# Kernel tuning notes

Measured on AMD Instinct MI355X. Metric: run time of the kernel, lower is better.

The kernel has to match this reference:

```python
import jax, jax.numpy as jnp
import numpy as np

N = 100000   # nodes per graph
E = 1200000  # edges per graph
D_IN = 64
FILTERS = [128, 128, 64]
K_SLICES = 16
MLP = [32, 16, 8, 4]


def setup_inputs() -> dict:
    key = jax.random.key(0)
    ks = jax.random.split(key, 24)
    s = 0.1
    inp = {
        'x_i': jax.random.normal(ks[0], (N, D_IN), jnp.float32),
        'edge_index_i': jax.random.randint(ks[1], (2, E), 0, N, jnp.int64),
        'x_j': jax.random.normal(ks[2], (N, D_IN), jnp.float32),
        'edge_index_j': jax.random.randint(ks[3], (2, E), 0, N, jnp.int64),
    }
    # GCN conv stack params: 64->128->128->64
    dims = [D_IN] + FILTERS
    for li in range(3):
        inp[f'conv_w{li}'] = jax.random.normal(ks[4 + 2 * li], (dims[li], dims[li + 1]), jnp.float32) * s
        inp[f'conv_b{li}'] = jnp.zeros((dims[li + 1],), jnp.float32)
    d = FILTERS[-1]
    inp['att_w'] = jax.random.normal(ks[10], (d, d), jnp.float32) * s
    inp['ntn_wt'] = jax.random.normal(ks[11], (K_SLICES, d, d), jnp.float32) * s
    inp['ntn_wm'] = jax.random.normal(ks[12], (K_SLICES, 2 * d), jnp.float32) * s
    inp['ntn_b'] = jnp.zeros((K_SLICES,), jnp.float32)
    mdims = [K_SLICES] + MLP
    for li in range(4):
        inp[f'mlp_w{li}'] = jax.random.normal(ks[13 + 2 * li], (mdims[li], mdims[li + 1]), jnp.float32) * s
        inp[f'mlp_b{li}'] = jnp.zeros((mdims[li + 1],), jnp.float32)
    inp['score_w'] = jax.random.normal(ks[22], (MLP[-1], 1), jnp.float32) * s
    inp['score_b'] = jnp.zeros((1,), jnp.float32)
    return inp


def _gcn(x, W, b, src, dst):
    # PyG GCNConv: add self loops, symmetric normalization, aggregate into dst.
    n = x.shape[0]
    loop = jnp.arange(n, dtype=src.dtype)
    src = jnp.concatenate([src, loop])
    dst = jnp.concatenate([dst, loop])
    deg = jax.ops.segment_sum(jnp.ones_like(dst, dtype=x.dtype), dst, num_segments=n)
    dinv = jax.lax.rsqrt(deg)  # deg >= 1 due to self loops
    norm = dinv[src] * dinv[dst]             # [E+N]
    xw = x @ W                               # [N, Dout]
    out = jax.ops.segment_sum(xw[src] * norm[:, None], dst, num_segments=n)
    return out + b


def _attention(x, Wa):
    # global context attention pooling over nodes
    gc = jnp.tanh(jnp.mean(x @ Wa, axis=0))          # [D]
    att = jax.nn.sigmoid(x @ gc)                     # [N]
    return jnp.sum(x * att[:, None], axis=0)         # [D]


def _ntn(h_i, h_j, Wt, Wm, b):
    # s_k = h_i^T Wt[k] h_j + Wm[k] . [h_i; h_j] + b_k, then tanh
    bilinear = jnp.einsum('d,kde,e->k', h_i, Wt, h_j)
    linear = Wm @ jnp.concatenate([h_i, h_j])
    return jnp.tanh(bilinear + linear + b)           # [K]


def reference(x_i, edge_index_i, x_j, edge_index_j,
              conv_w0, conv_b0, conv_w1, conv_b1, conv_w2, conv_b2,
              att_w, ntn_wt, ntn_wm, ntn_b,
              mlp_w0, mlp_b0, mlp_w1, mlp_b1, mlp_w2, mlp_b2, mlp_w3, mlp_b3,
              score_w, score_b):
    convs = [(conv_w0, conv_b0), (conv_w1, conv_b1), (conv_w2, conv_b2)]
    si, di = edge_index_i[0], edge_index_i[1]
    sj, dj = edge_index_j[0], edge_index_j[1]
    for li, (W, b) in enumerate(convs):
        x_i = _gcn(x_i, W, b, si, di)
        x_j = _gcn(x_j, W, b, sj, dj)
        if li < len(convs) - 1:
            x_i = jax.nn.relu(x_i)
            x_j = jax.nn.relu(x_j)
    h_i = _attention(x_i, att_w)
    h_j = _attention(x_j, att_w)
    z = _ntn(h_i, h_j, ntn_wt, ntn_wm, ntn_b)        # [K]
    for W, b in [(mlp_w0, mlp_b0), (mlp_w1, mlp_b1), (mlp_w2, mlp_b2), (mlp_w3, mlp_b3)]:
        z = jax.nn.relu(z @ W + b)
    return z @ score_w + score_b                     # [1]
```

## Files before the change

kernel.cpp:

```cpp
#include <hip/hip_runtime.h>
#include <cstdint>
#include <cstddef>

#define CDIV(a,b) (((a)+(b)-1)/(b))

typedef __attribute__((ext_vector_type(8))) unsigned short ushort8v;
typedef __attribute__((ext_vector_type(8))) short short8v;
typedef __attribute__((ext_vector_type(4))) float f32x4;

constexpr int BCAP = 8192;
constexpr int CPAD = 256 * BCAP;

__device__ __forceinline__ float bf2f(unsigned short u) {
  return __uint_as_float(((unsigned)u) << 16);
}
__device__ __forceinline__ unsigned short f2bf(float f) {
  unsigned u = __float_as_uint(f);
  unsigned r = (u + 0x7fff + ((u >> 16) & 1)) >> 16;
  return (unsigned short)r;
}


__global__ void k_prep(const float* __restrict__ w0, const float* __restrict__ w1,
                       const float* __restrict__ w2,
                       unsigned short* __restrict__ w0p, unsigned short* __restrict__ w1p,
                       unsigned short* __restrict__ w2p,
                       int* __restrict__ gcur, double* __restrict__ gcsum,
                       double* __restrict__ hsum) {
  int id = blockIdx.x * 256 + threadIdx.x;
  if (id < 512) gcur[id] = 0;
  else if (id < 640) gcsum[id - 512] = 0.0;
  else if (id < 768) hsum[id - 640] = 0.0;
  if (id < 8192) {
    int k = id / 128, n = id % 128;
    w0p[n * 64 + ((((k >> 3) + n) & 7) * 8) + (k & 7)] = f2bf(w0[id]);
  }
  if (id < 16384) {
    int k = id / 128, n = id % 128;
    w1p[n * 128 + ((((k >> 3) + n) & 15) * 8) + (k & 7)] = f2bf(w1[id]);
  }
  if (id < 8192) {
    int k = id / 64, n = id % 64;
    w2p[n * 128 + ((((k >> 3) + n) & 15) * 8) + (k & 7)] = f2bf(w2[id]);
  }
}


__global__ __launch_bounds__(256) void k_place(const int* __restrict__ src0,
                                               const int* __restrict__ dst0,
                                               const int* __restrict__ src1,
                                               const int* __restrict__ dst1,
                                               int E, int N,
                                               int* __restrict__ gcur,
                                               unsigned* __restrict__ part) {
  __shared__ int bcnt[256], bbase[256], bcur[256];
  int g = blockIdx.y;
  const int* src = g ? src1 : src0;
  const int* dst = g ? dst1 : dst0;
  int t = threadIdx.x;
  int e0 = blockIdx.x * 4096, e1 = min(e0 + 4096, E);
  bcnt[t] = 0;
  __syncthreads();
  for (int e = e0 + t; e < e1; e += 256) atomicAdd(&bcnt[dst[e] >> 9], 1);
  __syncthreads();
  bbase[t] = t * BCAP + (bcnt[t] ? atomicAdd(&gcur[g * 256 + t], bcnt[t]) : 0);
  bcur[t] = 0;
  __syncthreads();
  unsigned* pg = part + (size_t)g * CPAD;
  for (int e = e0 + t; e < e1; e += 256) {
    int d = dst[e], s = src[e];
    int b = d >> 9;
    int off = atomicAdd(&bcur[b], 1);
    pg[bbase[b] + off] = ((unsigned)(d & 511) << 18) | (unsigned)(s + g * N);
  }
}


__global__ __launch_bounds__(256) void k_build(const unsigned* __restrict__ part,
                                               const int* __restrict__ gcur,
                                               int2* __restrict__ rowp2, int* __restrict__ col,
                                               float* __restrict__ dinv, int n) {
  __shared__ int cnt[512], off[512], tmp[256];
  int g = blockIdx.y, b = blockIdx.x;
  int lo = b << 9;
  if (lo >= n) return;
  int t = threadIdx.x;
  int s0 = b * BCAP;
  int cntE = gcur[g * 256 + b];
  const unsigned* pg = part + (size_t)g * CPAD;
  cnt[t] = 0; cnt[t + 256] = 0;
  __syncthreads();
  for (int e = s0 + t; e < s0 + cntE; e += 256) atomicAdd(&cnt[pg[e] >> 18], 1);
  __syncthreads();
  int a0 = cnt[2 * t], a1 = cnt[2 * t + 1];
  int ps = a0 + a1;
  tmp[t] = ps; __syncthreads();
  for (int o = 1; o < 256; o <<= 1) {
    int x = (t >= o) ? tmp[t - o] : 0;
    __syncthreads();
    tmp[t] += x;
    __syncthreads();
  }
  int ex = tmp[t] - ps;
  off[2 * t] = ex;
  off[2 * t + 1] = ex + a0;
  __syncthreads();
  for (int i = t; i < 512; i += 256) {
    int node = lo + i;
    if (node < n) {
      int st = g * CPAD + s0 + off[i];
      rowp2[g * n + node] = make_int2(st, st + cnt[i]);
      dinv[g * n + node] = rsqrtf((float)(cnt[i] + 1));
    }
  }
  __syncthreads();
  for (int e = s0 + t; e < s0 + cntE; e += 256) {
    unsigned pr = pg[e];
    int p = atomicAdd(&off[pr >> 18], 1);
    col[g * CPAD + s0 + p] = (int)(pr & 0x3FFFFu);
  }
}


__global__ void k_tobf(const float* __restrict__ in0, const float* __restrict__ in1,
                       unsigned short* __restrict__ out, int n8half, int n8) {
  int i = blockIdx.x * blockDim.x + threadIdx.x;
  if (i < n8) {
    const float4* i4 = (i < n8half) ? (const float4*)in0 : (const float4*)in1;
    int ii = (i < n8half) ? i : i - n8half;
    float4 a = i4[2 * ii], b = i4[2 * ii + 1];
    ushort8v r;
    r[0] = f2bf(a.x); r[1] = f2bf(a.y); r[2] = f2bf(a.z); r[3] = f2bf(a.w);
    r[4] = f2bf(b.x); r[5] = f2bf(b.y); r[6] = f2bf(b.z); r[7] = f2bf(b.w);
    ((ushort8v*)out)[i] = r;
  }
}


template<int D, bool OUTBF, bool ADD_BIAS, bool COLSUM>
__device__ __forceinline__ void agg_body(
    const unsigned short* __restrict__ xin, void* __restrict__ xout,
    const int2* __restrict__ rowp2, const int* __restrict__ col,
    const float* __restrict__ dinv, const float* __restrict__ bias, int n,
    float* __restrict__ partial) {
  constexpr int G = D / 8;
  constexpr int NPB = 256 / G;
  int node = blockIdx.x * NPB + threadIdx.x / G;
  int g = threadIdx.x % G;
  const ushort8v* x8 = (const ushort8v*)xin;
  float r[8];
  bool valid = node < n;
  if (valid) {
    float di = dinv[node];
    float acc[8];
    {
      ushort8v xs = x8[(size_t)node * G + g];
#pragma unroll
      for (int j = 0; j < 8; ++j) acc[j] = di * bf2f(xs[j]);
    }
    int2 rp = rowp2[node];
    int e = rp.x, e1 = rp.y;
    for (; e + 8 <= e1; e += 8) {
      int s0 = col[e], s1 = col[e + 1], s2 = col[e + 2], s3 = col[e + 3];
      int s4 = col[e + 4], s5 = col[e + 5], s6 = col[e + 6], s7 = col[e + 7];
      float w0 = dinv[s0], w1 = dinv[s1], w2 = dinv[s2], w3 = dinv[s3];
      float w4 = dinv[s4], w5 = dinv[s5], w6 = dinv[s6], w7 = dinv[s7];
      ushort8v v0 = x8[(size_t)s0 * G + g];
      ushort8v v1 = x8[(size_t)s1 * G + g];
      ushort8v v2 = x8[(size_t)s2 * G + g];
      ushort8v v3 = x8[(size_t)s3 * G + g];
      ushort8v v4 = x8[(size_t)s4 * G + g];
      ushort8v v5 = x8[(size_t)s5 * G + g];
      ushort8v v6 = x8[(size_t)s6 * G + g];
      ushort8v v7 = x8[(size_t)s7 * G + g];
#pragma unroll
      for (int j = 0; j < 8; ++j) {
        acc[j] += w0 * bf2f(v0[j]); acc[j] += w1 * bf2f(v1[j]);
        acc[j] += w2 * bf2f(v2[j]); acc[j] += w3 * bf2f(v3[j]);
        acc[j] += w4 * bf2f(v4[j]); acc[j] += w5 * bf2f(v5[j]);
        acc[j] += w6 * bf2f(v6[j]); acc[j] += w7 * bf2f(v7[j]);
      }
    }
    for (; e + 4 <= e1; e += 4) {
      int s0 = col[e], s1 = col[e + 1], s2 = col[e + 2], s3 = col[e + 3];
      float w0 = dinv[s0], w1 = dinv[s1], w2 = dinv[s2], w3 = dinv[s3];
      ushort8v v0 = x8[(size_t)s0 * G + g];
      ushort8v v1 = x8[(size_t)s1 * G + g];
      ushort8v v2 = x8[(size_t)s2 * G + g];
      ushort8v v3 = x8[(size_t)s3 * G + g];
#pragma unroll
      for (int j = 0; j < 8; ++j) {
        acc[j] += w0 * bf2f(v0[j]); acc[j] += w1 * bf2f(v1[j]);
        acc[j] += w2 * bf2f(v2[j]); acc[j] += w3 * bf2f(v3[j]);
      }
    }
    for (; e < e1; ++e) {
      int s = col[e];
      float w = dinv[s];
      ushort8v v = x8[(size_t)s * G + g];
#pragma unroll
      for (int j = 0; j < 8; ++j) acc[j] += w * bf2f(v[j]);
    }
#pragma unroll
    for (int j = 0; j < 8; ++j) {
      r[j] = di * acc[j];
      if (ADD_BIAS) r[j] += bias[g * 8 + j];
    }
    if (OUTBF) {
      ushort8v o;
#pragma unroll
      for (int j = 0; j < 8; ++j) o[j] = f2bf(r[j]);
      ((ushort8v*)xout)[(size_t)node * G + g] = o;
    } else {
      float* op = (float*)xout + (size_t)node * D + g * 8;
      *(float4*)(op + 0) = make_float4(r[0], r[1], r[2], r[3]);
      *(float4*)(op + 4) = make_float4(r[4], r[5], r[6], r[7]);
    }
  } else {
#pragma unroll
    for (int j = 0; j < 8; ++j) r[j] = 0.f;
  }
  if (COLSUM) {
    __shared__ float ws[4][64];
    int lane = threadIdx.x & 63, wave = threadIdx.x >> 6;
#pragma unroll
    for (int j = 0; j < 8; ++j) {
      float v = r[j];
      v += __shfl_xor(v, 8);
      v += __shfl_xor(v, 16);
      v += __shfl_xor(v, 32);
      r[j] = v;
    }
    if (lane < 8) {
#pragma unroll
      for (int j = 0; j < 8; ++j) ws[wave][lane * 8 + j] = r[j];
    }
    __syncthreads();
    int t = threadIdx.x;
    if (t < 64) partial[(size_t)blockIdx.x * 64 + t] = ws[0][t] + ws[1][t] + ws[2][t] + ws[3][t];
  }
}

__global__ __launch_bounds__(256) void k_aggL0(
    const unsigned short* __restrict__ x, void* __restrict__ o,
    const int2* __restrict__ rp, const int* __restrict__ col,
    const float* __restrict__ dv, int n) {
  agg_body<64, true, false, false>(x, o, rp, col, dv, nullptr, n, nullptr);
}
__global__ __launch_bounds__(256) void k_aggL1(
    const unsigned short* __restrict__ x, void* __restrict__ o,
    const int2* __restrict__ rp, const int* __restrict__ col,
    const float* __restrict__ dv, int n) {
  agg_body<128, true, false, false>(x, o, rp, col, dv, nullptr, n, nullptr);
}
__global__ __launch_bounds__(256) void k_aggF(
    const unsigned short* __restrict__ x, void* __restrict__ o,
    const int2* __restrict__ rp, const int* __restrict__ col,
    const float* __restrict__ dv, const float* __restrict__ bias, int n,
    float* __restrict__ partial) {
  agg_body<64, false, true, true>(x, o, rp, col, dv, bias, n, partial);
}


template<int K, int DOUT, bool RELU>
__device__ __forceinline__ void gemm_body(
    const unsigned short* __restrict__ A, const unsigned short* __restrict__ Wp,
    const float* __restrict__ bias, unsigned short* __restrict__ C, int n) {
  constexpr int CPR = K / 8;
  constexpr int CM = CPR - 1;
  constexpr int NT = DOUT / 16;
  __shared__ unsigned short As[128 * K];
  __shared__ unsigned short Ws[DOUT * K];
  int t = threadIdx.x;
  int blockM = blockIdx.x * 128;

#pragma unroll
  for (int id = t; id < 128 * CPR; id += 256) {
    int r = id / CPR, c = id % CPR;
    int grow = blockM + r;
    ushort8v v = {0, 0, 0, 0, 0, 0, 0, 0};
    if (grow < n) v = ((const ushort8v*)A)[(size_t)grow * CPR + c];
    *(ushort8v*)&As[r * K + ((c + r) & CM) * 8] = v;
  }
#pragma unroll
  for (int id = t; id < DOUT * CPR; id += 256)
    ((ushort8v*)Ws)[id] = ((const ushort8v*)Wp)[id];
  __syncthreads();

  int lane = t & 63, wave = t >> 6;
  int m15 = lane & 15, quad = lane >> 4;
  f32x4 acc[2][NT];
#pragma unroll
  for (int i = 0; i < 2; ++i)
#pragma unroll
    for (int j = 0; j < NT; ++j) acc[i][j] = (f32x4){0.f, 0.f, 0.f, 0.f};

  int i0 = wave * 32 + m15;
  int i1 = i0 + 16;
#pragma unroll
  for (int kc = 0; kc < K; kc += 32) {
    int c0 = (kc >> 3) + quad;
    short8v a0 = *(const short8v*)&As[i0 * K + ((c0 + i0) & CM) * 8];
    short8v a1 = *(const short8v*)&As[i1 * K + ((c0 + i1) & CM) * 8];
    short8v b[NT];
#pragma unroll
    for (int nt = 0; nt < NT; ++nt) {
      int nn = nt * 16 + m15;
      b[nt] = *(const short8v*)&Ws[nn * K + ((c0 + nn) & CM) * 8];
    }
#pragma unroll
    for (int nt = 0; nt < NT; ++nt) {
      acc[0][nt] = __builtin_amdgcn_mfma_f32_16x16x32_bf16(a0, b[nt], acc[0][nt], 0, 0, 0);
      acc[1][nt] = __builtin_amdgcn_mfma_f32_16x16x32_bf16(a1, b[nt], acc[1][nt], 0, 0, 0);
    }
  }

#pragma unroll
  for (int rt = 0; rt < 2; ++rt) {
    int rbase = blockM + wave * 32 + rt * 16 + quad * 4;
#pragma unroll
    for (int nt = 0; nt < NT; ++nt) {
      int colg = nt * 16 + m15;
      float bv = bias ? bias[colg] : 0.f;
#pragma unroll
      for (int r = 0; r < 4; ++r) {
        int row = rbase + r;
        if (row < n) {
          float v = acc[rt][nt][r] + bv;
          if (RELU) v = fmaxf(v, 0.f);
          C[(size_t)row * DOUT + colg] = f2bf(v);
        }
      }
    }
  }
}

__global__ __launch_bounds__(256) void k_gemmL0(
    const unsigned short* __restrict__ A, const unsigned short* __restrict__ Wp,
    const float* __restrict__ bias, unsigned short* __restrict__ C, int n) {
  gemm_body<64, 128, true>(A, Wp, bias, C, n);
}
__global__ __launch_bounds__(256) void k_gemmL1(
    const unsigned short* __restrict__ A, const unsigned short* __restrict__ Wp,
    const float* __restrict__ bias, unsigned short* __restrict__ C, int n) {
  gemm_body<128, 128, true>(A, Wp, bias, C, n);
}
__global__ __launch_bounds__(256) void k_gemmL2(
    const unsigned short* __restrict__ A, const unsigned short* __restrict__ Wp,
    const float* __restrict__ bias, unsigned short* __restrict__ C, int n) {
  gemm_body<128, 64, false>(A, Wp, bias, C, n);
}


__global__ __launch_bounds__(256) void k_cm2(const float* __restrict__ partial, int nbg,
                                             double* __restrict__ gcsum) {
  __shared__ double sd[256];
  int g = blockIdx.y, t = threadIdx.x;
  int f = t & 63, rg = t >> 6;
  double acc = 0.0;
  for (int b = blockIdx.x * 4 + rg; b < nbg; b += gridDim.x * 4)
    acc += (double)partial[(size_t)(g * nbg + b) * 64 + f];
  sd[t] = acc; __syncthreads();
  if (t < 64) {
    double tot = sd[t] + sd[t + 64] + sd[t + 128] + sd[t + 192];
    atomicAdd(&gcsum[g * 64 + t], tot);
  }
}


__global__ void k_hsum(const float* __restrict__ x, const double* __restrict__ gcsum,
                       const float* __restrict__ Wa, int N, int n2,
                       double* __restrict__ hsum) {
  __shared__ float m[128], gcs[128];
  __shared__ double sd[256][4];
  int t = threadIdx.x;
  if (t < 128) m[t] = (float)(gcsum[t] / (double)N);
  __syncthreads();
  if (t < 128) {
    int gg = t >> 6, f = t & 63;
    float s = 0.f;
    for (int d = 0; d < 64; ++d) s += m[gg * 64 + d] * Wa[d * 64 + f];
    gcs[t] = tanhf(s);
  }
  __syncthreads();
  int g = t & 15, sub = t >> 4;
  float4 gcv0 = ((const float4*)gcs)[g];
  float4 gcv1 = ((const float4*)gcs)[16 + g];
  double a[2][4];
#pragma unroll
  for (int j = 0; j < 4; ++j) { a[0][j] = 0.0; a[1][j] = 0.0; }
  for (int node = blockIdx.x * 16 + sub; node < n2; node += gridDim.x * 16) {
    int gid = node >= N;
    float4 gcv = gid ? gcv1 : gcv0;
    float4 xv = ((const float4*)x)[(size_t)node * 16 + g];
    float p = xv.x * gcv.x + xv.y * gcv.y + xv.z * gcv.z + xv.w * gcv.w;
    p += __shfl_xor(p, 1);
    p += __shfl_xor(p, 2);
    p += __shfl_xor(p, 4);
    p += __shfl_xor(p, 8);
    float att = 1.f / (1.f + expf(-p));
    a[gid][0] += (double)(att * xv.x); a[gid][1] += (double)(att * xv.y);
    a[gid][2] += (double)(att * xv.z); a[gid][3] += (double)(att * xv.w);
  }
#pragma unroll 1
  for (int gid = 0; gid < 2; ++gid) {
    sd[t][0] = a[gid][0]; sd[t][1] = a[gid][1];
    sd[t][2] = a[gid][2]; sd[t][3] = a[gid][3];
    __syncthreads();
    if (t < 64) {
      int gg = t >> 2, j = t & 3;
      double tot = 0;
      for (int w = 0; w < 16; ++w) tot += sd[w * 16 + gg][j];
      if (tot != 0.0) atomicAdd(&hsum[gid * 64 + t], tot);
    }
    __syncthreads();
  }
}


__global__ __launch_bounds__(1024) void k_final(
    const double* __restrict__ hsum,
    const float* __restrict__ Wt, const float* __restrict__ Wm,
    const float* __restrict__ bn,
    const float* __restrict__ w0, const float* __restrict__ b0,
    const float* __restrict__ w1, const float* __restrict__ b1,
    const float* __restrict__ w2, const float* __restrict__ b2,
    const float* __restrict__ w3, const float* __restrict__ b3,
    const float* __restrict__ sw, const float* __restrict__ sb,
    float* __restrict__ out) {
  __shared__ float hi[64], hj[64], red[1024], z[16], u[32], v[16], w[8], q[4];
  int t = threadIdx.x;
  if (t < 64) hi[t] = (float)hsum[t];
  else if (t < 128) hj[t - 64] = (float)hsum[t];
  __syncthreads();
  int k = t >> 6, r = t & 63;
  const float* wr = Wt + ((size_t)k * 64 + r) * 64;
  float s = 0.f;
#pragma unroll 8
  for (int c = 0; c < 64; ++c) s += wr[c] * hj[c];
  float p = hi[r] * s;
  p += Wm[k * 128 + r] * hi[r] + Wm[k * 128 + 64 + r] * hj[r];
  red[t] = p;
  __syncthreads();
  for (int o = 32; o > 0; o >>= 1) {
    if (r < o) red[t] += red[t + o];
    __syncthreads();
  }
  if (t < 16) z[t] = tanhf(red[t * 64] + bn[t]);
  __syncthreads();
  if (t < 32) {
    float ss = b0[t];
    for (int i = 0; i < 16; ++i) ss += z[i] * w0[i * 32 + t];
    u[t] = fmaxf(ss, 0.f);
  }
  __syncthreads();
  if (t < 16) {
    float ss = b1[t];
    for (int i = 0; i < 32; ++i) ss += u[i] * w1[i * 16 + t];
    v[t] = fmaxf(ss, 0.f);
  }
  __syncthreads();
  if (t < 8) {
    float ss = b2[t];
    for (int i = 0; i < 16; ++i) ss += v[i] * w2[i * 8 + t];
    w[t] = fmaxf(ss, 0.f);
  }
  __syncthreads();
  if (t < 4) {
    float ss = b3[t];
    for (int i = 0; i < 8; ++i) ss += w[i] * w3[i * 4 + t];
    q[t] = fmaxf(ss, 0.f);
  }
  __syncthreads();
  if (t == 0) {
    float ss = sb[0];
    for (int i = 0; i < 4; ++i) ss += q[i] * sw[i];
    out[0] = ss;
  }
}


extern "C" void kernel_launch(void* const* d_in, const int* in_sizes, int n_in,
                              void* d_out, int out_size, void* d_ws, size_t ws_size,
                              hipStream_t stream) {
  const float* x_i = (const float*)d_in[0];
  const int*   ei  = (const int*)d_in[1];
  const float* x_j = (const float*)d_in[2];
  const int*   ej  = (const int*)d_in[3];
  const float* cw0 = (const float*)d_in[4];  const float* cb0 = (const float*)d_in[5];
  const float* cw1 = (const float*)d_in[6];  const float* cb1 = (const float*)d_in[7];
  const float* cw2 = (const float*)d_in[8];  const float* cb2 = (const float*)d_in[9];
  const float* aw  = (const float*)d_in[10];
  const float* wt  = (const float*)d_in[11]; const float* wm  = (const float*)d_in[12];
  const float* bn  = (const float*)d_in[13];
  const float* m0w = (const float*)d_in[14]; const float* m0b = (const float*)d_in[15];
  const float* m1w = (const float*)d_in[16]; const float* m1b = (const float*)d_in[17];
  const float* m2w = (const float*)d_in[18]; const float* m2b = (const float*)d_in[19];
  const float* m3w = (const float*)d_in[20]; const float* m3b = (const float*)d_in[21];
  const float* sw  = (const float*)d_in[22]; const float* sb  = (const float*)d_in[23];

  int N = in_sizes[0] / 64;
  int E = in_sizes[1] / 2;
  int N2 = 2 * N;

  char* p = (char*)d_ws;
  auto alloc = [&](size_t b) -> void* {
    void* r = (void*)p;
    p += (b + 255) & ~(size_t)255;
    return r;
  };
  int*    gcur    = (int*)alloc(512 * 4);
  double* gcsum   = (double*)alloc(128 * 8);
  double* hsum    = (double*)alloc(128 * 8);
  int2*   rowp2   = (int2*)alloc((size_t)N2 * 8);
  int*    col     = (int*)alloc((size_t)2 * CPAD * 4);
  float*  dinv    = (float*)alloc((size_t)N2 * 4);
  float*  partial = (float*)alloc((size_t)CDIV(N2, 32) * 64 * 4);
  unsigned short* w0p = (unsigned short*)alloc(64 * 128 * 2);
  unsigned short* w1p = (unsigned short*)alloc(128 * 128 * 2);
  unsigned short* w2p = (unsigned short*)alloc(128 * 64 * 2);
  char* S1 = (char*)alloc((size_t)N2 * 128 * 2);
  char* S2 = (char*)alloc((size_t)N2 * 128 * 2);

  k_prep<<<64, 256, 0, stream>>>(cw0, cw1, cw2, w0p, w1p, w2p, gcur, gcsum, hsum);

  unsigned* part = (unsigned*)S1;
  k_place<<<dim3(CDIV(E, 4096), 2), 256, 0, stream>>>(ei, ei + E, ej, ej + E, E, N, gcur, part);
  k_build<<<dim3(256, 2), 256, 0, stream>>>(part, gcur, rowp2, col, dinv, N);

  unsigned short* xbf = (unsigned short*)S2;
  k_tobf<<<CDIV(N2 * 8, 256), 256, 0, stream>>>(x_i, x_j, xbf, N * 8, N2 * 8);

  unsigned short* A0 = (unsigned short*)S1;
  unsigned short* G0 = (unsigned short*)S2;
  unsigned short* A1 = (unsigned short*)S1;
  unsigned short* G1 = (unsigned short*)S2;
  unsigned short* G2 = (unsigned short*)S1;
  float* F = (float*)S2;

  k_aggL0<<<CDIV(N2, 32), 256, 0, stream>>>(xbf, A0, rowp2, col, dinv, N2);
  k_gemmL0<<<CDIV(N2, 128), 256, 0, stream>>>(A0, w0p, cb0, G0, N2);
  k_aggL1<<<CDIV(N2, 16), 256, 0, stream>>>(G0, A1, rowp2, col, dinv, N2);
  k_gemmL1<<<CDIV(N2, 128), 256, 0, stream>>>(A1, w1p, cb1, G1, N2);
  k_gemmL2<<<CDIV(N2, 128), 256, 0, stream>>>(G1, w2p, nullptr, G2, N2);
  k_aggF<<<CDIV(N2, 32), 256, 0, stream>>>(G2, F, rowp2, col, dinv, cb2, N2, partial);

  k_cm2<<<dim3(32, 2), 256, 0, stream>>>(partial, N / 32, gcsum);
  k_hsum<<<1024, 256, 0, stream>>>(F, gcsum, aw, N, N2, hsum);

  k_final<<<1, 1024, 0, stream>>>(hsum, wt, wm, bn,
                                  m0w, m0b, m1w, m1b, m2w, m2b, m3w, m3b,
                                  sw, sb, (float*)d_out);
}
```

Baseline: 578.4 us.

## Prescale features by source dinv to drop per-edge dinv gathers; store final output bf16

Folds the source-side normalization dinv[src] into the producers: the bf16 conversion and the GEMM epilogues multiply each row by its dinv before storing. The aggregation kernels then sum neighbor rows without weights, which removes one random gather per edge. The edge loop is also reduced from an 8-way to a 4-way unroll. The final aggregated features are written as bf16 instead of fp32, and the attention kernel reads bf16, which halves that traffic but adds rounding error before pooling.

```diff
diff --git a/kernel.cpp b/kernel.cpp
--- a/kernel.cpp
+++ b/kernel.cpp
@@ -123,23 +123,25 @@
 
 
 __global__ void k_tobf(const float* __restrict__ in0, const float* __restrict__ in1,
+                       const float* __restrict__ dinv,
                        unsigned short* __restrict__ out, int n8half, int n8) {
   int i = blockIdx.x * blockDim.x + threadIdx.x;
   if (i < n8) {
     const float4* i4 = (i < n8half) ? (const float4*)in0 : (const float4*)in1;
     int ii = (i < n8half) ? i : i - n8half;
+    float di = dinv[i >> 3];
     float4 a = i4[2 * ii], b = i4[2 * ii + 1];
     ushort8v r;
-    r[0] = f2bf(a.x); r[1] = f2bf(a.y); r[2] = f2bf(a.z); r[3] = f2bf(a.w);
-    r[4] = f2bf(b.x); r[5] = f2bf(b.y); r[6] = f2bf(b.z); r[7] = f2bf(b.w);
+    r[0] = f2bf(di * a.x); r[1] = f2bf(di * a.y); r[2] = f2bf(di * a.z); r[3] = f2bf(di * a.w);
+    r[4] = f2bf(di * b.x); r[5] = f2bf(di * b.y); r[6] = f2bf(di * b.z); r[7] = f2bf(di * b.w);
     ((ushort8v*)out)[i] = r;
   }
 }
 
 
-template<int D, bool OUTBF, bool ADD_BIAS, bool COLSUM>
+template<int D, bool ADD_BIAS, bool COLSUM>
 __device__ __forceinline__ void agg_body(
-    const unsigned short* __restrict__ xin, void* __restrict__ xout,
+    const unsigned short* __restrict__ xin, unsigned short* __restrict__ xout,
     const int2* __restrict__ rowp2, const int* __restrict__ col,
     const float* __restrict__ dinv, const float* __restrict__ bias, int n,
     float* __restrict__ partial) {
@@ -149,73 +151,43 @@
   int g = threadIdx.x % G;
   const ushort8v* x8 = (const ushort8v*)xin;
   float r[8];
-  bool valid = node < n;
-  if (valid) {
+  if (node < n) {
     float di = dinv[node];
     float acc[8];
     {
       ushort8v xs = x8[(size_t)node * G + g];
 #pragma unroll
-      for (int j = 0; j < 8; ++j) acc[j] = di * bf2f(xs[j]);
+      for (int j = 0; j < 8; ++j) acc[j] = bf2f(xs[j]);
     }
     int2 rp = rowp2[node];
     int e = rp.x, e1 = rp.y;
-    for (; e + 8 <= e1; e += 8) {
+    for (; e + 4 <= e1; e += 4) {
       int s0 = col[e], s1 = col[e + 1], s2 = col[e + 2], s3 = col[e + 3];
-      int s4 = col[e + 4], s5 = col[e + 5], s6 = col[e + 6], s7 = col[e + 7];
-      float w0 = dinv[s0], w1 = dinv[s1], w2 = dinv[s2], w3 = dinv[s3];
-      float w4 = dinv[s4], w5 = dinv[s5], w6 = dinv[s6], w7 = dinv[s7];
       ushort8v v0 = x8[(size_t)s0 * G + g];
       ushort8v v1 = x8[(size_t)s1 * G + g];
       ushort8v v2 = x8[(size_t)s2 * G + g];
       ushort8v v3 = x8[(size_t)s3 * G + g];
-      ushort8v v4 = x8[(size_t)s4 * G + g];
-      ushort8v v5 = x8[(size_t)s5 * G + g];
-      ushort8v v6 = x8[(size_t)s6 * G + g];
-      ushort8v v7 = x8[(size_t)s7 * G + g];
 #pragma unroll
       for (int j = 0; j < 8; ++j) {
-        acc[j] += w0 * bf2f(v0[j]); acc[j] += w1 * bf2f(v1[j]);
-        acc[j] += w2 * bf2f(v2[j]); acc[j] += w3 * bf2f(v3[j]);
-        acc[j] += w4 * bf2f(v4[j]); acc[j] += w5 * bf2f(v5[j]);
-        acc[j] += w6 * bf2f(v6[j]); acc[j] += w7 * bf2f(v7[j]);
-      }
-    }
-    for (; e + 4 <= e1; e += 4) {
-      int s0 = col[e], s1 = col[e + 1], s2 = col[e + 2], s3 = col[e + 3];
-      float w0 = dinv[s0], w1 = dinv[s1], w2 = dinv[s2], w3 = dinv[s3];
-      ushort8v v0 = x8[(size_t)s0 * G + g];
-      ushort8v v1 = x8[(size_t)s1 * G + g];
-      ushort8v v2 = x8[(size_t)s2 * G + g];
-      ushort8v v3 = x8[(size_t)s3 * G + g];
-#pragma unroll
-      for (int j = 0; j < 8; ++j) {
-        acc[j] += w0 * bf2f(v0[j]); acc[j] += w1 * bf2f(v1[j]);
-        acc[j] += w2 * bf2f(v2[j]); acc[j] += w3 * bf2f(v3[j]);
+        acc[j] += bf2f(v0[j]); acc[j] += bf2f(v1[j]);
+        acc[j] += bf2f(v2[j]); acc[j] += bf2f(v3[j]);
       }
     }
     for (; e < e1; ++e) {
       int s = col[e];
-      float w = dinv[s];
       ushort8v v = x8[(size_t)s * G + g];
 #pragma unroll
-      for (int j = 0; j < 8; ++j) acc[j] += w * bf2f(v[j]);
+      for (int j = 0; j < 8; ++j) acc[j] += bf2f(v[j]);
     }
 #pragma unroll
     for (int j = 0; j < 8; ++j) {
       r[j] = di * acc[j];
       if (ADD_BIAS) r[j] += bias[g * 8 + j];
     }
-    if (OUTBF) {
-      ushort8v o;
-#pragma unroll
-      for (int j = 0; j < 8; ++j) o[j] = f2bf(r[j]);
-      ((ushort8v*)xout)[(size_t)node * G + g] = o;
-    } else {
-      float* op = (float*)xout + (size_t)node * D + g * 8;
-      *(float4*)(op + 0) = make_float4(r[0], r[1], r[2], r[3]);
-      *(float4*)(op + 4) = make_float4(r[4], r[5], r[6], r[7]);
-    }
+    ushort8v o;
+#pragma unroll
+    for (int j = 0; j < 8; ++j) o[j] = f2bf(r[j]);
+    ((ushort8v*)xout)[(size_t)node * G + g] = o;
   } else {
 #pragma unroll
     for (int j = 0; j < 8; ++j) r[j] = 0.f;
@@ -242,30 +214,31 @@
 }
 
 __global__ __launch_bounds__(256) void k_aggL0(
-    const unsigned short* __restrict__ x, void* __restrict__ o,
+    const unsigned short* __restrict__ x, unsigned short* __restrict__ o,
     const int2* __restrict__ rp, const int* __restrict__ col,
     const float* __restrict__ dv, int n) {
-  agg_body<64, true, false, false>(x, o, rp, col, dv, nullptr, n, nullptr);
+  agg_body<64, false, false>(x, o, rp, col, dv, nullptr, n, nullptr);
 }
 __global__ __launch_bounds__(256) void k_aggL1(
-    const unsigned short* __restrict__ x, void* __restrict__ o,
+    const unsigned short* __restrict__ x, unsigned short* __restrict__ o,
     const int2* __restrict__ rp, const int* __restrict__ col,
     const float* __restrict__ dv, int n) {
-  agg_body<128, true, false, false>(x, o, rp, col, dv, nullptr, n, nullptr);
+  agg_body<128, false, false>(x, o, rp, col, dv, nullptr, n, nullptr);
 }
 __global__ __launch_bounds__(256) void k_aggF(
-    const unsigned short* __restrict__ x, void* __restrict__ o,
+    const unsigned short* __restrict__ x, unsigned short* __restrict__ o,
     const int2* __restrict__ rp, const int* __restrict__ col,
     const float* __restrict__ dv, const float* __restrict__ bias, int n,
     float* __restrict__ partial) {
-  agg_body<64, false, true, true>(x, o, rp, col, dv, bias, n, partial);
-}
-
-
-template<int K, int DOUT, bool RELU>
+  agg_body<64, true, true>(x, o, rp, col, dv, bias, n, partial);
+}
+
+
+template<int K, int DOUT, bool RELU, bool PRESCALE>
 __device__ __forceinline__ void gemm_body(
     const unsigned short* __restrict__ A, const unsigned short* __restrict__ Wp,
-    const float* __restrict__ bias, unsigned short* __restrict__ C, int n) {
+    const float* __restrict__ bias, unsigned short* __restrict__ C,
+    const float* __restrict__ dinv, int n) {
   constexpr int CPR = K / 8;
   constexpr int CM = CPR - 1;
   constexpr int NT = DOUT / 16;
@@ -328,6 +301,7 @@
         if (row < n) {
           float v = acc[rt][nt][r] + bv;
           if (RELU) v = fmaxf(v, 0.f);
+          if (PRESCALE) v *= dinv[row];
           C[(size_t)row * DOUT + colg] = f2bf(v);
         }
       }
@@ -337,18 +311,21 @@
 
 __global__ __launch_bounds__(256) void k_gemmL0(
     const unsigned short* __restrict__ A, const unsigned short* __restrict__ Wp,
-    const float* __restrict__ bias, unsigned short* __restrict__ C, int n) {
-  gemm_body<64, 128, true>(A, Wp, bias, C, n);
+    const float* __restrict__ bias, unsigned short* __restrict__ C,
+    const float* __restrict__ dv, int n) {
+  gemm_body<64, 128, true, true>(A, Wp, bias, C, dv, n);
 }
 __global__ __launch_bounds__(256) void k_gemmL1(
     const unsigned short* __restrict__ A, const unsigned short* __restrict__ Wp,
-    const float* __restrict__ bias, unsigned short* __restrict__ C, int n) {
-  gemm_body<128, 128, true>(A, Wp, bias, C, n);
+    const float* __restrict__ bias, unsigned short* __restrict__ C,
+    const float* __restrict__ dv, int n) {
+  gemm_body<128, 128, true, false>(A, Wp, bias, C, dv, n);
 }
 __global__ __launch_bounds__(256) void k_gemmL2(
     const unsigned short* __restrict__ A, const unsigned short* __restrict__ Wp,
-    const float* __restrict__ bias, unsigned short* __restrict__ C, int n) {
-  gemm_body<128, 64, false>(A, Wp, bias, C, n);
+    const float* __restrict__ bias, unsigned short* __restrict__ C,
+    const float* __restrict__ dv, int n) {
+  gemm_body<128, 64, false, true>(A, Wp, bias, C, dv, n);
 }
 
 
@@ -368,7 +345,7 @@
 }
 
 
-__global__ void k_hsum(const float* __restrict__ x, const double* __restrict__ gcsum,
+__global__ void k_hsum(const unsigned short* __restrict__ x, const double* __restrict__ gcsum,
                        const float* __restrict__ Wa, int N, int n2,
                        double* __restrict__ hsum) {
   __shared__ float m[128], gcs[128];
@@ -392,15 +369,16 @@
   for (int node = blockIdx.x * 16 + sub; node < n2; node += gridDim.x * 16) {
     int gid = node >= N;
     float4 gcv = gid ? gcv1 : gcv0;
-    float4 xv = ((const float4*)x)[(size_t)node * 16 + g];
-    float p = xv.x * gcv.x + xv.y * gcv.y + xv.z * gcv.z + xv.w * gcv.w;
+    ushort4 xu = ((const ushort4*)x)[(size_t)node * 16 + g];
+    float x0 = bf2f(xu.x), x1 = bf2f(xu.y), x2 = bf2f(xu.z), x3 = bf2f(xu.w);
+    float p = x0 * gcv.x + x1 * gcv.y + x2 * gcv.z + x3 * gcv.w;
     p += __shfl_xor(p, 1);
     p += __shfl_xor(p, 2);
     p += __shfl_xor(p, 4);
     p += __shfl_xor(p, 8);
     float att = 1.f / (1.f + expf(-p));
-    a[gid][0] += (double)(att * xv.x); a[gid][1] += (double)(att * xv.y);
-    a[gid][2] += (double)(att * xv.z); a[gid][3] += (double)(att * xv.w);
+    a[gid][0] += (double)(att * x0); a[gid][1] += (double)(att * x1);
+    a[gid][2] += (double)(att * x2); a[gid][3] += (double)(att * x3);
   }
 #pragma unroll 1
   for (int gid = 0; gid < 2; ++gid) {
@@ -529,20 +507,20 @@
   k_build<<<dim3(256, 2), 256, 0, stream>>>(part, gcur, rowp2, col, dinv, N);
 
   unsigned short* xbf = (unsigned short*)S2;
-  k_tobf<<<CDIV(N2 * 8, 256), 256, 0, stream>>>(x_i, x_j, xbf, N * 8, N2 * 8);
+  k_tobf<<<CDIV(N2 * 8, 256), 256, 0, stream>>>(x_i, x_j, dinv, xbf, N * 8, N2 * 8);
 
   unsigned short* A0 = (unsigned short*)S1;
   unsigned short* G0 = (unsigned short*)S2;
   unsigned short* A1 = (unsigned short*)S1;
   unsigned short* G1 = (unsigned short*)S2;
   unsigned short* G2 = (unsigned short*)S1;
-  float* F = (float*)S2;
+  unsigned short* F = (unsigned short*)S2;
 
   k_aggL0<<<CDIV(N2, 32), 256, 0, stream>>>(xbf, A0, rowp2, col, dinv, N2);
-  k_gemmL0<<<CDIV(N2, 128), 256, 0, stream>>>(A0, w0p, cb0, G0, N2);
+  k_gemmL0<<<CDIV(N2, 128), 256, 0, stream>>>(A0, w0p, cb0, G0, dinv, N2);
   k_aggL1<<<CDIV(N2, 16), 256, 0, stream>>>(G0, A1, rowp2, col, dinv, N2);
-  k_gemmL1<<<CDIV(N2, 128), 256, 0, stream>>>(A1, w1p, cb1, G1, N2);
-  k_gemmL2<<<CDIV(N2, 128), 256, 0, stream>>>(G1, w2p, nullptr, G2, N2);
+  k_gemmL1<<<CDIV(N2, 128), 256, 0, stream>>>(A1, w1p, cb1, G1, dinv, N2);
+  k_gemmL2<<<CDIV(N2, 128), 256, 0, stream>>>(G1, w2p, nullptr, G2, dinv, N2);
   k_aggF<<<CDIV(N2, 32), 256, 0, stream>>>(G2, F, rowp2, col, dinv, cb2, N2, partial);
 
   k_cm2<<<dim3(32, 2), 256, 0, stream>>>(partial, N / 32, gcsum);
```

Measured after the change: 565.1 us. 1.02x faster.
